# Kernel tuning notes

Hardware: AMD Instinct MI355X
Metric: run time of the kernel (lower is better)

The kernel has to match this reference:

```python
import jax, jax.numpy as jnp
import numpy as np

ALPHA = 0.5      # GCN2Conv alpha
THETA = 1.0      # GCN2Conv theta (beta_l = log(theta/l + 1))
EPS = 1e-5       # pyg LayerNorm eps
N_LAYERS = 8
N, E, DIN, DHID, DOUT = 50000, 800000, 128, 256, 128


def setup_inputs() -> dict:
    key = jax.random.key(0)
    ks = jax.random.split(key, 10)
    x = jax.random.normal(ks[0], (N, DIN), jnp.float32)
    edge_index = jax.random.randint(ks[1], (2, E), 0, N, dtype=jnp.int32)
    lin1_w = jax.random.normal(ks[2], (DIN, DHID), jnp.float32) / np.sqrt(DIN)
    lin1_b = jnp.zeros((DHID,), jnp.float32)
    conv_w1 = jax.random.normal(ks[3], (N_LAYERS, DHID, DHID), jnp.float32) / np.sqrt(DHID)
    conv_w2 = jax.random.normal(ks[4], (N_LAYERS, DHID, DHID), jnp.float32) / np.sqrt(DHID)
    norm_gamma = jnp.ones((N_LAYERS, DHID), jnp.float32)
    norm_beta = jnp.zeros((N_LAYERS, DHID), jnp.float32)
    lin2_w = jax.random.normal(ks[5], (DHID, DOUT), jnp.float32) / np.sqrt(DHID)
    lin2_b = jnp.zeros((DOUT,), jnp.float32)
    return {"x": x, "edge_index": edge_index, "lin1_w": lin1_w, "lin1_b": lin1_b,
            "conv_w1": conv_w1, "conv_w2": conv_w2, "norm_gamma": norm_gamma,
            "norm_beta": norm_beta, "lin2_w": lin2_w, "lin2_b": lin2_b}


def _gcn_norm(edge_index, n_nodes, dtype):
    # add self loops, then symmetric deg^{-1/2} A_hat deg^{-1/2} normalization
    loop = jnp.arange(n_nodes, dtype=edge_index.dtype)
    row = jnp.concatenate([edge_index[0], loop])
    col = jnp.concatenate([edge_index[1], loop])
    deg = jax.ops.segment_sum(jnp.ones_like(row, dtype=dtype), col, num_segments=n_nodes)
    dis = jnp.where(deg > 0, jax.lax.rsqrt(jnp.maximum(deg, 1e-12)), 0.0)
    return row, col, dis[row] * dis[col]


def _graph_layernorm(h, gamma, beta):
    # pyg LayerNorm mode='graph', batch=None: normalize over all nodes+features
    z = h - jnp.mean(h)
    z = z / (jnp.sqrt(jnp.mean(z * z)) + EPS)
    return gamma * z + beta


def reference(x, edge_index, lin1_w, lin1_b, conv_w1, conv_w2, norm_gamma, norm_beta, lin2_w, lin2_b):
    n_nodes = x.shape[0]
    row, col, enorm = _gcn_norm(edge_index, n_nodes, x.dtype)
    # lin1 + relu (dropout p=0 -> identity); residual=None -> zeros
    x0 = jax.nn.relu(x @ lin1_w + lin1_b)
    h = x0
    for i in range(conv_w1.shape[0]):
        beta_l = float(np.log(THETA / (i + 1) + 1.0))
        # sparse neighborhood aggregation: out[c] += norm * h[r]
        agg = jax.ops.segment_sum(h[row] * enorm[:, None], col, num_segments=n_nodes)
        t = (1.0 - ALPHA) * agg          # propagated part
        r = ALPHA * x0                   # initial-residual part (res = x0 + zeros)
        # shared_weights=False: separate weights for propagated and residual parts
        h = (1.0 - beta_l) * (t + r) + beta_l * (t @ conv_w1[i] + r @ conv_w2[i])
        h = jax.nn.relu(_graph_layernorm(h, norm_gamma[i], norm_beta[i]))
    return jax.nn.relu(h @ lin2_w + lin2_b)
```

## Files before the change

kernel.cpp:

```cpp
#include <hip/hip_runtime.h>
#include <hip/hip_bf16.h>
#include <math.h>

#define DIN 128
#define DH 256
#define DOUT 128
#define NLAYERS 8
#define EPSLN 1e-5f

typedef __hip_bfloat16 bf16;
typedef __attribute__((ext_vector_type(8))) short short8;
typedef __attribute__((ext_vector_type(4))) short short4v;
typedef __attribute__((ext_vector_type(4))) float f32x4;

__device__ __forceinline__ float ldf(const void* p, size_t idx, int isbf) {
    if (isbf) return __bfloat162float(((const bf16*)p)[idx]);
    return ((const float*)p)[idx];
}
__device__ __forceinline__ short f2s(float v) {
    bf16 b = __float2bfloat16(v);
    return *reinterpret_cast<short*>(&b);
}
__device__ __forceinline__ float s2f(short s) {
    unsigned int u = ((unsigned int)(unsigned short)s) << 16;
    float f;
    __builtin_memcpy(&f, &u, 4);
    return f;
}
__device__ __forceinline__ void gl_lds16(const void* g, void* l) {
    __builtin_amdgcn_global_load_lds(
        (const __attribute__((address_space(1))) unsigned int*)g,
        (__attribute__((address_space(3))) unsigned int*)l,
        16, 0, 0);
}

__global__ void k_detect(const unsigned int* __restrict__ xw, int* __restrict__ flag) {
    __shared__ int cnt;
    if (threadIdx.x == 0) cnt = 0;
    __syncthreads();
    unsigned int w = xw[threadIdx.x];
    int e = (w >> 7) & 0xFF;
    if (e >= 112 && e <= 140) atomicAdd(&cnt, 1);
    __syncthreads();
    if (threadIdx.x == 0) *flag = (cnt >= 128) ? 1 : 0;
}

__global__ void k_init_cnt(int* __restrict__ cnt, int N) {
    int i = blockIdx.x * blockDim.x + threadIdx.x;
    if (i < N) cnt[i] = 0;
}
__global__ void k_count(const int* __restrict__ cols, int* __restrict__ cnt, int E) {
    int e = blockIdx.x * blockDim.x + threadIdx.x;
    if (e < E) atomicAdd(&cnt[cols[e]], 1);
}
__global__ void k_dis(const int* __restrict__ cnt, float* __restrict__ dis, int N) {
    int i = blockIdx.x * blockDim.x + threadIdx.x;
    if (i < N) dis[i] = rsqrtf(1.0f + (float)cnt[i]);
}
__global__ void k_scan1(const int* __restrict__ cnt, int* __restrict__ rowptr,
                        int* __restrict__ bsum, int N) {
    __shared__ int s[256];
    int t = threadIdx.x;
    int i = blockIdx.x * 256 + t;
    s[t] = (i < N) ? cnt[i] : 0;
    __syncthreads();
    for (int off = 1; off < 256; off <<= 1) {
        int x = (t >= off) ? s[t - off] : 0;
        __syncthreads();
        s[t] += x;
        __syncthreads();
    }
    if (i < N) rowptr[i + 1] = s[t];
    if (t == 255) bsum[blockIdx.x] = s[255];
}
__global__ void k_scan2(int* __restrict__ bsum, int nb) {
    __shared__ int s[256];
    int t = threadIdx.x;
    s[t] = (t < nb) ? bsum[t] : 0;
    __syncthreads();
    for (int off = 1; off < 256; off <<= 1) {
        int x = (t >= off) ? s[t - off] : 0;
        __syncthreads();
        s[t] += x;
        __syncthreads();
    }
    if (t < nb) bsum[t] = s[t];
}
__global__ void k_scan3(int* __restrict__ rowptr, const int* __restrict__ bsum, int N) {
    int i = blockIdx.x * 256 + threadIdx.x;
    if (i == 0) rowptr[0] = 0;
    if (i < N && blockIdx.x > 0) rowptr[i + 1] += bsum[blockIdx.x - 1];
}
__global__ void k_cursor(const int* __restrict__ rowptr, int* __restrict__ cursor, int N) {
    int i = blockIdx.x * 256 + threadIdx.x;
    if (i < N) cursor[i] = rowptr[i];
}
__global__ void k_fill(const int* __restrict__ rows, const int* __restrict__ cols,
                       int* __restrict__ cursor, int* __restrict__ csr, int E) {
    int e = blockIdx.x * blockDim.x + threadIdx.x;
    if (e < E) {
        int c = cols[e], r = rows[e];
        int pos = atomicAdd(&cursor[c], 1);
        csr[pos] = r;
    }
}

__global__ void k_zero_stats(float* __restrict__ stats) {
    int t = threadIdx.x;
    if (t < 16) stats[t] = 0.0f;
}

__global__ void k_transw2(const void* __restrict__ w1, const void* __restrict__ w2,
                          const int* __restrict__ flag, short* __restrict__ wt) {
    __shared__ float tile[32][33];
    int z = blockIdx.z;
    int lay = z >> 1, m = z & 1;
    const void* src = m ? w2 : w1;
    size_t sbase = (size_t)lay * 65536;
    short* dst = wt + (size_t)lay * 131072 + (size_t)m * 256;
    float bl = logf(1.0f / (float)(lay + 1) + 1.0f);
    float c0 = 0.5f * (1.0f - bl);
    float c1 = 0.5f * bl;
    int isbf = *flag;
    int tx = threadIdx.x, ty = threadIdx.y;
    int n0 = blockIdx.x * 32, k0 = blockIdx.y * 32;
    #pragma unroll
    for (int i = 0; i < 4; i++) {
        int k = k0 + ty + i * 8;
        tile[ty + i * 8][tx] = ldf(src, sbase + (size_t)k * 256 + n0 + tx, isbf);
    }
    __syncthreads();
    #pragma unroll
    for (int i = 0; i < 4; i++) {
        int n = n0 + ty + i * 8;
        int k = k0 + tx;
        float v = c1 * tile[tx][ty + i * 8];
        if (k == n) v += c0;
        dst[(size_t)n * 512 + k] = f2s(v);
    }
}

__global__ void k_transw_lin(const void* __restrict__ src, const int* __restrict__ flag,
                             short* __restrict__ dst, int K, int Nc) {
    __shared__ float tile[32][33];
    int isbf = *flag;
    int tx = threadIdx.x, ty = threadIdx.y;
    int n0 = blockIdx.x * 32, k0 = blockIdx.y * 32;
    #pragma unroll
    for (int i = 0; i < 4; i++) {
        int k = k0 + ty + i * 8;
        tile[ty + i * 8][tx] = ldf(src, (size_t)k * Nc + n0 + tx, isbf);
    }
    __syncthreads();
    #pragma unroll
    for (int i = 0; i < 4; i++) {
        int n = n0 + ty + i * 8;
        dst[(size_t)n * K + k0 + tx] = f2s(tile[tx][ty + i * 8]);
    }
}

__global__ void k_convx(const void* __restrict__ x, const int* __restrict__ flag,
                        short* __restrict__ xb, int total) {
    int i = blockIdx.x * 256 + threadIdx.x;
    if (i < total) xb[i] = f2s(ldf(x, i, *flag));
}

template<int KK, int FINAL>
__global__ __launch_bounds__(256) void gemm_mfma(
    const short* __restrict__ A, const short* __restrict__ wt,
    const void* __restrict__ bias, const int* __restrict__ flag,
    void* __restrict__ outp, int Nn)
{
    __shared__ __align__(16) short Atile[128 * 32];
    __shared__ __align__(16) short Btile[128 * 32];
    int t = threadIdx.x;
    int w = t >> 6, lane = t & 63;
    int lr = lane & 15, quad = lane >> 4;
    int row0 = blockIdx.x * 128;
    int col0 = blockIdx.y * 128;
    int ncols = gridDim.y * 128;
    int sub = t & 3;
    int srow = t >> 2;
    f32x4 acc[2][8];
    #pragma unroll
    for (int m = 0; m < 2; m++)
        #pragma unroll
        for (int nt = 0; nt < 8; nt++)
            #pragma unroll
            for (int j = 0; j < 4; j++) acc[m][nt][j] = 0.f;

    for (int kb = 0; kb < KK; kb += 32) {
        #pragma unroll
        for (int r = 0; r < 2; r++) {
            int gr = row0 + srow + r * 64;
            if (gr >= Nn) gr = Nn - 1;
            gl_lds16(A + (size_t)gr * KK + kb + sub * 8,
                     Atile + (size_t)(t + r * 256) * 8);
        }
        #pragma unroll
        for (int r = 0; r < 2; r++) {
            int n = col0 + srow + r * 64;
            gl_lds16(wt + (size_t)n * KK + kb + sub * 8,
                     Btile + (size_t)(t + r * 256) * 8);
        }
        __syncthreads();
        short8 a0 = *(const short8*)(Atile + (w * 32 + lr) * 32 + quad * 8);
        short8 a1 = *(const short8*)(Atile + (w * 32 + 16 + lr) * 32 + quad * 8);
        #pragma unroll
        for (int nt = 0; nt < 8; nt++) {
            short8 bv = *(const short8*)(Btile + (nt * 16 + lr) * 32 + quad * 8);
            acc[0][nt] = __builtin_amdgcn_mfma_f32_16x16x32_bf16(a0, bv, acc[0][nt], 0, 0, 0);
            acc[1][nt] = __builtin_amdgcn_mfma_f32_16x16x32_bf16(a1, bv, acc[1][nt], 0, 0, 0);
        }
        __syncthreads();
    }
    const int isbf = *flag;
    #pragma unroll
    for (int m = 0; m < 2; m++) {
        #pragma unroll
        for (int nt = 0; nt < 8; nt++) {
            int gc = col0 + nt * 16 + lr;
            float bb = ldf(bias, gc, isbf);
            #pragma unroll
            for (int i = 0; i < 4; i++) {
                int gr = row0 + w * 32 + m * 16 + quad * 4 + i;
                if (gr < Nn) {
                    float v = acc[m][nt][i] + bb;
                    v = v > 0.f ? v : 0.f;
                    size_t off = (size_t)gr * ncols + gc;
                    if (FINAL) {
                        if (isbf) ((bf16*)outp)[off] = __float2bfloat16(v);
                        else      ((float*)outp)[off] = v;
                    } else {
                        ((bf16*)outp)[off] = __float2bfloat16(v);
                    }
                }
            }
        }
    }
}

__global__ __launch_bounds__(256) void k_gather4(
    const int* __restrict__ rowptr, const int* __restrict__ csr,
    const float* __restrict__ dis, const bf16* __restrict__ hsrc,
    bf16* __restrict__ agg, int N)
{
    int gid = blockIdx.x * 256 + threadIdx.x;
    int node = gid >> 6;
    if (node >= N) return;
    int col = (gid & 63) * 4;
    const short* hs = (const short*)hsrc;
    float dc = dis[node];
    float a0[4], a1[4], a2[4], a3[4];
    {
        short4v hv = *(const short4v*)(hs + (size_t)node * DH + col);
        #pragma unroll
        for (int j = 0; j < 4; j++) {
            a0[j] = dc * s2f(hv[j]);
            a1[j] = 0.f; a2[j] = 0.f; a3[j] = 0.f;
        }
    }
    int i = rowptr[node], e1 = rowptr[node + 1];
    for (; i + 8 <= e1; i += 8) {
        int r0 = csr[i],     r1 = csr[i + 1], r2 = csr[i + 2], r3 = csr[i + 3];
        int r4 = csr[i + 4], r5 = csr[i + 5], r6 = csr[i + 6], r7 = csr[i + 7];
        float w0 = dis[r0], w1 = dis[r1], w2 = dis[r2], w3 = dis[r3];
        float w4 = dis[r4], w5 = dis[r5], w6 = dis[r6], w7 = dis[r7];
        short4v v0 = *(const short4v*)(hs + (size_t)r0 * DH + col);
        short4v v1 = *(const short4v*)(hs + (size_t)r1 * DH + col);
        short4v v2 = *(const short4v*)(hs + (size_t)r2 * DH + col);
        short4v v3 = *(const short4v*)(hs + (size_t)r3 * DH + col);
        short4v v4 = *(const short4v*)(hs + (size_t)r4 * DH + col);
        short4v v5 = *(const short4v*)(hs + (size_t)r5 * DH + col);
        short4v v6 = *(const short4v*)(hs + (size_t)r6 * DH + col);
        short4v v7 = *(const short4v*)(hs + (size_t)r7 * DH + col);
        #pragma unroll
        for (int j = 0; j < 4; j++) {
            a0[j] = fmaf(w0, s2f(v0[j]), a0[j]);
            a1[j] = fmaf(w1, s2f(v1[j]), a1[j]);
            a2[j] = fmaf(w2, s2f(v2[j]), a2[j]);
            a3[j] = fmaf(w3, s2f(v3[j]), a3[j]);
            a0[j] = fmaf(w4, s2f(v4[j]), a0[j]);
            a1[j] = fmaf(w5, s2f(v5[j]), a1[j]);
            a2[j] = fmaf(w6, s2f(v6[j]), a2[j]);
            a3[j] = fmaf(w7, s2f(v7[j]), a3[j]);
        }
    }
    for (; i + 2 <= e1; i += 2) {
        int r0 = csr[i], r1 = csr[i + 1];
        float w0 = dis[r0], w1 = dis[r1];
        short4v v0 = *(const short4v*)(hs + (size_t)r0 * DH + col);
        short4v v1 = *(const short4v*)(hs + (size_t)r1 * DH + col);
        #pragma unroll
        for (int j = 0; j < 4; j++) {
            a0[j] = fmaf(w0, s2f(v0[j]), a0[j]);
            a1[j] = fmaf(w1, s2f(v1[j]), a1[j]);
        }
    }
    for (; i < e1; i++) {
        int r = csr[i];
        float wr = dis[r];
        short4v v0 = *(const short4v*)(hs + (size_t)r * DH + col);
        #pragma unroll
        for (int j = 0; j < 4; j++) a0[j] = fmaf(wr, s2f(v0[j]), a0[j]);
    }
    short4v o;
    #pragma unroll
    for (int j = 0; j < 4; j++) o[j] = f2s(dc * ((a0[j] + a1[j]) + (a2[j] + a3[j])));
    *(short4v*)((short*)agg + (size_t)node * DH + col) = o;
}

__global__ __launch_bounds__(256) void gemm_layer4(
    const bf16* __restrict__ agg, const bf16* __restrict__ x0,
    const short* __restrict__ wt, bf16* __restrict__ h,
    float* __restrict__ stats2, int Nn)
{
    __shared__ __align__(16) short Atile[128 * 32];
    __shared__ __align__(16) short Btile[128 * 32];
    __shared__ float red[512];
    int t = threadIdx.x;
    int w = t >> 6, lane = t & 63;
    int lr = lane & 15, quad = lane >> 4;
    int row0 = blockIdx.x * 128;
    int col0 = blockIdx.y * 128;
    int sub = t & 3;
    int srow = t >> 2;
    f32x4 acc[2][8];
    #pragma unroll
    for (int m = 0; m < 2; m++)
        #pragma unroll
        for (int nt = 0; nt < 8; nt++)
            #pragma unroll
            for (int j = 0; j < 4; j++) acc[m][nt][j] = 0.f;

    for (int kb = 0; kb < 512; kb += 32) {
        const short* Asrc = (const short*)((kb < DH) ? agg : x0);
        int ka = kb & (DH - 1);
        #pragma unroll
        for (int r = 0; r < 2; r++) {
            int gr = row0 + srow + r * 64;
            if (gr >= Nn) gr = Nn - 1;
            gl_lds16(Asrc + (size_t)gr * DH + ka + sub * 8,
                     Atile + (size_t)(t + r * 256) * 8);
        }
        #pragma unroll
        for (int r = 0; r < 2; r++) {
            int n = col0 + srow + r * 64;
            gl_lds16(wt + (size_t)n * 512 + kb + sub * 8,
                     Btile + (size_t)(t + r * 256) * 8);
        }
        __syncthreads();
        short8 a0 = *(const short8*)(Atile + (w * 32 + lr) * 32 + quad * 8);
        short8 a1 = *(const short8*)(Atile + (w * 32 + 16 + lr) * 32 + quad * 8);
        #pragma unroll
        for (int nt = 0; nt < 8; nt++) {
            short8 bv = *(const short8*)(Btile + (nt * 16 + lr) * 32 + quad * 8);
            acc[0][nt] = __builtin_amdgcn_mfma_f32_16x16x32_bf16(a0, bv, acc[0][nt], 0, 0, 0);
            acc[1][nt] = __builtin_amdgcn_mfma_f32_16x16x32_bf16(a1, bv, acc[1][nt], 0, 0, 0);
        }
        __syncthreads();
    }
    float lsum = 0.f, lsq = 0.f;
    #pragma unroll
    for (int m = 0; m < 2; m++) {
        #pragma unroll
        for (int nt = 0; nt < 8; nt++) {
            int gc = col0 + nt * 16 + lr;
            #pragma unroll
            for (int i = 0; i < 4; i++) {
                int gr = row0 + w * 32 + m * 16 + quad * 4 + i;
                if (gr < Nn) {
                    float v = acc[m][nt][i];
                    h[(size_t)gr * DH + gc] = __float2bfloat16(v);
                    lsum += v;
                    lsq += v * v;
                }
            }
        }
    }
    red[t] = lsum;
    red[256 + t] = lsq;
    __syncthreads();
    for (int s = 128; s > 0; s >>= 1) {
        if (t < s) { red[t] += red[t + s]; red[256 + t] += red[256 + t + s]; }
        __syncthreads();
    }
    if (t == 0) {
        atomicAdd(&stats2[0], red[0]);
        atomicAdd(&stats2[1], red[256]);
    }
}

__global__ __launch_bounds__(256) void k_applyT(
    bf16* __restrict__ h, const float* __restrict__ stats2, float invTotal,
    const void* __restrict__ g, const void* __restrict__ b, size_t loff,
    const int* __restrict__ flag, int total)
{
    int idx = blockIdx.x * 256 + threadIdx.x;
    if (idx >= total) return;
    const int isbf = *flag;
    float mu = stats2[0] * invTotal;
    float var = stats2[1] * invTotal - mu * mu;
    var = var > 0.f ? var : 0.f;
    float inv = 1.0f / (sqrtf(var) + EPSLN);
    int j = idx & (DH - 1);
    float gg = ldf(g, loff + j, isbf);
    float bb = ldf(b, loff + j, isbf);
    float v = fmaf(gg * inv, __bfloat162float(h[idx]), fmaf(-gg * inv, mu, bb));
    v = v > 0.f ? v : 0.f;
    h[idx] = __float2bfloat16(v);
}

extern "C" void kernel_launch(void* const* d_in, const int* in_sizes, int n_in,
                              void* d_out, int out_size, void* d_ws, size_t ws_size,
                              hipStream_t stream) {
    const void* x      = d_in[0];
    const int*  ei     = (const int*)d_in[1];
    const void* lin1_w = d_in[2];
    const void* lin1_b = d_in[3];
    const void* conv_w1= d_in[4];
    const void* conv_w2= d_in[5];
    const void* gam    = d_in[6];
    const void* bet    = d_in[7];
    const void* lin2_w = d_in[8];
    const void* lin2_b = d_in[9];

    const int N = in_sizes[0] / DIN;
    const int E = in_sizes[1] / 2;
    const int* rows = ei;
    const int* cols = ei + E;
    const size_t NDH = (size_t)N * DH;
    const size_t Nr = ((size_t)N + 255) / 256 * 256;

    char* p = (char*)d_ws;
    auto alloc = [&](size_t bytes) { char* q = p; p += (bytes + 255) & ~(size_t)255; return q; };
    float* dis    = (float*)alloc(Nr * 4);
    float* stats  = (float*)alloc(1024);
    int*   flag   = (int*)(stats + 16);
    int*   cnt    = (int*)alloc(Nr * 4);
    int*   rowptr = (int*)alloc((Nr + 256) * 4);
    int*   cursor = (int*)alloc(Nr * 4);
    int*   bsum   = (int*)alloc(1024);
    int*   csr    = (int*)alloc((size_t)E * 4);
    short* wt     = (short*)alloc((size_t)NLAYERS * 131072 * 2);
    short* w1t    = (short*)alloc((size_t)DH * DIN * 2);
    short* w2t    = (short*)alloc((size_t)DOUT * DH * 2);
    short* xb     = (short*)alloc((size_t)N * DIN * 2);
    bf16*  agg    = (bf16*)alloc(NDH * 2);
    bf16*  x0     = (bf16*)alloc(NDH * 2);
    bf16*  h      = (bf16*)alloc(NDH * 2);

    dim3 blk(256);
    int nbN = (N + 255) / 256;
    dim3 gN(nbN);
    dim3 gE((E + 255) / 256);
    dim3 gB128_2((N + 127) / 128, 2);
    dim3 gB128_1((N + 127) / 128, 1);
    dim3 gG((N + 3) / 4);
    dim3 gElem((unsigned)((NDH + 255) / 256));
    dim3 gTW(8, 8, 16);
    dim3 bTW(32, 8);

    k_detect<<<1, 256, 0, stream>>>((const unsigned int*)x, flag);
    k_init_cnt<<<gN, blk, 0, stream>>>(cnt, N);
    k_count<<<gE, blk, 0, stream>>>(cols, cnt, E);
    k_dis<<<gN, blk, 0, stream>>>(cnt, dis, N);
    k_scan1<<<gN, blk, 0, stream>>>(cnt, rowptr, bsum, N);
    k_scan2<<<1, 256, 0, stream>>>(bsum, nbN);
    k_scan3<<<gN, blk, 0, stream>>>(rowptr, bsum, N);
    k_cursor<<<gN, blk, 0, stream>>>(rowptr, cursor, N);
    k_fill<<<gE, blk, 0, stream>>>(rows, cols, cursor, csr, E);
    k_zero_stats<<<1, 64, 0, stream>>>(stats);
    k_transw2<<<gTW, bTW, 0, stream>>>(conv_w1, conv_w2, flag, wt);
    k_transw_lin<<<dim3(DH / 32, DIN / 32), bTW, 0, stream>>>(lin1_w, flag, w1t, DIN, DH);
    k_transw_lin<<<dim3(DOUT / 32, DH / 32), bTW, 0, stream>>>(lin2_w, flag, w2t, DH, DOUT);
    k_convx<<<dim3((unsigned)(((size_t)N * DIN + 255) / 256)), blk, 0, stream>>>(x, flag, xb, N * DIN);

    gemm_mfma<DIN, 0><<<gB128_2, blk, 0, stream>>>(xb, w1t, lin1_b, flag, x0, N);

    const float invTotal = 1.0f / ((float)N * (float)DH);
    for (int l = 0; l < NLAYERS; l++) {
        const bf16* hsrc = (l == 0) ? x0 : h;
        if (l > 0) {
            k_applyT<<<gElem, blk, 0, stream>>>(h, stats + 2 * (l - 1), invTotal,
                                                gam, bet, (size_t)(l - 1) * DH,
                                                flag, (int)NDH);
        }
        k_gather4<<<gG, blk, 0, stream>>>(rowptr, csr, dis, hsrc, agg, N);
        gemm_layer4<<<gB128_2, blk, 0, stream>>>(agg, x0, wt + (size_t)l * 131072,
                                                 h, stats + 2 * l, N);
    }
    k_applyT<<<gElem, blk, 0, stream>>>(h, stats + 2 * (NLAYERS - 1), invTotal,
                                        gam, bet, (size_t)(NLAYERS - 1) * DH,
                                        flag, (int)NDH);
    gemm_mfma<DH, 1><<<gB128_1, blk, 0, stream>>>((const short*)h, w2t, lin2_b,
                                                  flag, d_out, N);
}
```

Baseline: 1.329 ms.

## Fuse graph LayerNorm+ReLU into gather and final GEMM, drop apply pass

Removes the separate k_applyT elementwise pass over h. The LayerNorm affine and ReLU are now applied on the fly to each neighbor row read in the gather kernel, and while loading A tiles in the final GEMM. It also merges the cursor init into scan3 and the stats zeroing into init_cnt, cutting launches. The catch is that normalization is recomputed for every edge read (about 17 per node) instead of once per element. The final GEMM also switches from async global-to-LDS loads to register loads with per-element gamma/beta fetches.

```diff
diff --git a/kernel.cpp b/kernel.cpp
--- a/kernel.cpp
+++ b/kernel.cpp
@@ -45,9 +45,10 @@
     if (threadIdx.x == 0) *flag = (cnt >= 128) ? 1 : 0;
 }
 
-__global__ void k_init_cnt(int* __restrict__ cnt, int N) {
+__global__ void k_init_cnt(int* __restrict__ cnt, float* __restrict__ stats, int N) {
     int i = blockIdx.x * blockDim.x + threadIdx.x;
     if (i < N) cnt[i] = 0;
+    if (blockIdx.x == 0 && threadIdx.x < 16) stats[threadIdx.x] = 0.0f;
 }
 __global__ void k_count(const int* __restrict__ cols, int* __restrict__ cnt, int E) {
     int e = blockIdx.x * blockDim.x + threadIdx.x;
@@ -86,14 +87,15 @@
     }
     if (t < nb) bsum[t] = s[t];
 }
-__global__ void k_scan3(int* __restrict__ rowptr, const int* __restrict__ bsum, int N) {
+__global__ void k_scan3(int* __restrict__ rowptr, const int* __restrict__ bsum,
+                        int* __restrict__ cursor, int N) {
     int i = blockIdx.x * 256 + threadIdx.x;
-    if (i == 0) rowptr[0] = 0;
-    if (i < N && blockIdx.x > 0) rowptr[i + 1] += bsum[blockIdx.x - 1];
-}
-__global__ void k_cursor(const int* __restrict__ rowptr, int* __restrict__ cursor, int N) {
-    int i = blockIdx.x * 256 + threadIdx.x;
-    if (i < N) cursor[i] = rowptr[i];
+    if (i == 0) { rowptr[0] = 0; cursor[0] = 0; }
+    if (i < N) {
+        int v = rowptr[i + 1] + ((blockIdx.x > 0) ? bsum[blockIdx.x - 1] : 0);
+        rowptr[i + 1] = v;
+        cursor[i + 1] = v;
+    }
 }
 __global__ void k_fill(const int* __restrict__ rows, const int* __restrict__ cols,
                        int* __restrict__ cursor, int* __restrict__ csr, int E) {
@@ -103,11 +105,6 @@
         int pos = atomicAdd(&cursor[c], 1);
         csr[pos] = r;
     }
-}
-
-__global__ void k_zero_stats(float* __restrict__ stats) {
-    int t = threadIdx.x;
-    if (t < 16) stats[t] = 0.0f;
 }
 
 __global__ void k_transw2(const void* __restrict__ w1, const void* __restrict__ w2,
@@ -165,10 +162,12 @@
     if (i < total) xb[i] = f2s(ldf(x, i, *flag));
 }
 
-template<int KK, int FINAL>
+template<int KK, int FINAL, int TRANSA>
 __global__ __launch_bounds__(256) void gemm_mfma(
     const short* __restrict__ A, const short* __restrict__ wt,
     const void* __restrict__ bias, const int* __restrict__ flag,
+    const void* __restrict__ g, const void* __restrict__ b, size_t loff,
+    const float* __restrict__ stats2, float invTotal,
     void* __restrict__ outp, int Nn)
 {
     __shared__ __align__(16) short Atile[128 * 32];
@@ -181,6 +180,14 @@
     int ncols = gridDim.y * 128;
     int sub = t & 3;
     int srow = t >> 2;
+    const int isbf = *flag;
+    float mu = 0.f, inv = 0.f;
+    if (TRANSA) {
+        mu = stats2[0] * invTotal;
+        float var = stats2[1] * invTotal - mu * mu;
+        var = var > 0.f ? var : 0.f;
+        inv = 1.0f / (sqrtf(var) + EPSLN);
+    }
     f32x4 acc[2][8];
     #pragma unroll
     for (int m = 0; m < 2; m++)
@@ -194,8 +201,23 @@
         for (int r = 0; r < 2; r++) {
             int gr = row0 + srow + r * 64;
             if (gr >= Nn) gr = Nn - 1;
-            gl_lds16(A + (size_t)gr * KK + kb + sub * 8,
-                     Atile + (size_t)(t + r * 256) * 8);
+            if (TRANSA) {
+                short8 av = *(const short8*)(A + (size_t)gr * KK + kb + sub * 8);
+                short8 tv;
+                #pragma unroll
+                for (int j = 0; j < 8; j++) {
+                    int kc = kb + sub * 8 + j;
+                    float gg = ldf(g, loff + kc, isbf);
+                    float bb = ldf(b, loff + kc, isbf);
+                    float v = fmaf(gg * inv, s2f(av[j]), fmaf(-gg * inv, mu, bb));
+                    v = v > 0.f ? v : 0.f;
+                    tv[j] = f2s(v);
+                }
+                *(short8*)(Atile + (size_t)(t + r * 256) * 8) = tv;
+            } else {
+                gl_lds16(A + (size_t)gr * KK + kb + sub * 8,
+                         Atile + (size_t)(t + r * 256) * 8);
+            }
         }
         #pragma unroll
         for (int r = 0; r < 2; r++) {
@@ -214,7 +236,6 @@
         }
         __syncthreads();
     }
-    const int isbf = *flag;
     #pragma unroll
     for (int m = 0; m < 2; m++) {
         #pragma unroll
@@ -240,15 +261,36 @@
     }
 }
 
-__global__ __launch_bounds__(256) void k_gather4(
+__global__ __launch_bounds__(256) void k_gather5(
     const int* __restrict__ rowptr, const int* __restrict__ csr,
     const float* __restrict__ dis, const bf16* __restrict__ hsrc,
-    bf16* __restrict__ agg, int N)
+    bf16* __restrict__ agg,
+    const void* __restrict__ g, const void* __restrict__ b, size_t loff,
+    const float* __restrict__ stats2, float invTotal, int useLN,
+    const int* __restrict__ flag, int N)
 {
     int gid = blockIdx.x * 256 + threadIdx.x;
     int node = gid >> 6;
     if (node >= N) return;
     int col = (gid & 63) * 4;
+    float cA[4], cB[4];
+    if (useLN) {
+        int isbf = *flag;
+        float mu = stats2[0] * invTotal;
+        float var = stats2[1] * invTotal - mu * mu;
+        var = var > 0.f ? var : 0.f;
+        float inv = 1.0f / (sqrtf(var) + EPSLN);
+        #pragma unroll
+        for (int j = 0; j < 4; j++) {
+            float gg = ldf(g, loff + col + j, isbf);
+            float bb = ldf(b, loff + col + j, isbf);
+            cA[j] = gg * inv;
+            cB[j] = fmaf(-gg * inv, mu, bb);
+        }
+    } else {
+        #pragma unroll
+        for (int j = 0; j < 4; j++) { cA[j] = 1.0f; cB[j] = 0.0f; }
+    }
     const short* hs = (const short*)hsrc;
     float dc = dis[node];
     float a0[4], a1[4], a2[4], a3[4];
@@ -256,7 +298,9 @@
         short4v hv = *(const short4v*)(hs + (size_t)node * DH + col);
         #pragma unroll
         for (int j = 0; j < 4; j++) {
-            a0[j] = dc * s2f(hv[j]);
+            float v = fmaf(cA[j], s2f(hv[j]), cB[j]);
+            v = v > 0.f ? v : 0.f;
+            a0[j] = dc * v;
             a1[j] = 0.f; a2[j] = 0.f; a3[j] = 0.f;
         }
     }
@@ -276,14 +320,22 @@
         short4v v7 = *(const short4v*)(hs + (size_t)r7 * DH + col);
         #pragma unroll
         for (int j = 0; j < 4; j++) {
-            a0[j] = fmaf(w0, s2f(v0[j]), a0[j]);
-            a1[j] = fmaf(w1, s2f(v1[j]), a1[j]);
-            a2[j] = fmaf(w2, s2f(v2[j]), a2[j]);
-            a3[j] = fmaf(w3, s2f(v3[j]), a3[j]);
-            a0[j] = fmaf(w4, s2f(v4[j]), a0[j]);
-            a1[j] = fmaf(w5, s2f(v5[j]), a1[j]);
-            a2[j] = fmaf(w6, s2f(v6[j]), a2[j]);
-            a3[j] = fmaf(w7, s2f(v7[j]), a3[j]);
+            float t0 = fmaf(cA[j], s2f(v0[j]), cB[j]); t0 = t0 > 0.f ? t0 : 0.f;
+            float t1 = fmaf(cA[j], s2f(v1[j]), cB[j]); t1 = t1 > 0.f ? t1 : 0.f;
+            float t2 = fmaf(cA[j], s2f(v2[j]), cB[j]); t2 = t2 > 0.f ? t2 : 0.f;
+            float t3 = fmaf(cA[j], s2f(v3[j]), cB[j]); t3 = t3 > 0.f ? t3 : 0.f;
+            float t4 = fmaf(cA[j], s2f(v4[j]), cB[j]); t4 = t4 > 0.f ? t4 : 0.f;
+            float t5 = fmaf(cA[j], s2f(v5[j]), cB[j]); t5 = t5 > 0.f ? t5 : 0.f;
+            float t6 = fmaf(cA[j], s2f(v6[j]), cB[j]); t6 = t6 > 0.f ? t6 : 0.f;
+            float t7 = fmaf(cA[j], s2f(v7[j]), cB[j]); t7 = t7 > 0.f ? t7 : 0.f;
+            a0[j] = fmaf(w0, t0, a0[j]);
+            a1[j] = fmaf(w1, t1, a1[j]);
+            a2[j] = fmaf(w2, t2, a2[j]);
+            a3[j] = fmaf(w3, t3, a3[j]);
+            a0[j] = fmaf(w4, t4, a0[j]);
+            a1[j] = fmaf(w5, t5, a1[j]);
+            a2[j] = fmaf(w6, t6, a2[j]);
+            a3[j] = fmaf(w7, t7, a3[j]);
         }
     }
     for (; i + 2 <= e1; i += 2) {
@@ -293,8 +345,10 @@
         short4v v1 = *(const short4v*)(hs + (size_t)r1 * DH + col);
         #pragma unroll
         for (int j = 0; j < 4; j++) {
-            a0[j] = fmaf(w0, s2f(v0[j]), a0[j]);
-            a1[j] = fmaf(w1, s2f(v1[j]), a1[j]);
+            float t0 = fmaf(cA[j], s2f(v0[j]), cB[j]); t0 = t0 > 0.f ? t0 : 0.f;
+            float t1 = fmaf(cA[j], s2f(v1[j]), cB[j]); t1 = t1 > 0.f ? t1 : 0.f;
+            a0[j] = fmaf(w0, t0, a0[j]);
+            a1[j] = fmaf(w1, t1, a1[j]);
         }
     }
     for (; i < e1; i++) {
@@ -302,7 +356,10 @@
         float wr = dis[r];
         short4v v0 = *(const short4v*)(hs + (size_t)r * DH + col);
         #pragma unroll
-        for (int j = 0; j < 4; j++) a0[j] = fmaf(wr, s2f(v0[j]), a0[j]);
+        for (int j = 0; j < 4; j++) {
+            float t0 = fmaf(cA[j], s2f(v0[j]), cB[j]); t0 = t0 > 0.f ? t0 : 0.f;
+            a0[j] = fmaf(wr, t0, a0[j]);
+        }
     }
     short4v o;
     #pragma unroll
@@ -391,26 +448,6 @@
     }
 }
 
-__global__ __launch_bounds__(256) void k_applyT(
-    bf16* __restrict__ h, const float* __restrict__ stats2, float invTotal,
-    const void* __restrict__ g, const void* __restrict__ b, size_t loff,
-    const int* __restrict__ flag, int total)
-{
-    int idx = blockIdx.x * 256 + threadIdx.x;
-    if (idx >= total) return;
-    const int isbf = *flag;
-    float mu = stats2[0] * invTotal;
-    float var = stats2[1] * invTotal - mu * mu;
-    var = var > 0.f ? var : 0.f;
-    float inv = 1.0f / (sqrtf(var) + EPSLN);
-    int j = idx & (DH - 1);
-    float gg = ldf(g, loff + j, isbf);
-    float bb = ldf(b, loff + j, isbf);
-    float v = fmaf(gg * inv, __bfloat162float(h[idx]), fmaf(-gg * inv, mu, bb));
-    v = v > 0.f ? v : 0.f;
-    h[idx] = __float2bfloat16(v);
-}
-
 extern "C" void kernel_launch(void* const* d_in, const int* in_sizes, int n_in,
                               void* d_out, int out_size, void* d_ws, size_t ws_size,
                               hipStream_t stream) {
@@ -439,7 +476,7 @@
     int*   flag   = (int*)(stats + 16);
     int*   cnt    = (int*)alloc(Nr * 4);
     int*   rowptr = (int*)alloc((Nr + 256) * 4);
-    int*   cursor = (int*)alloc(Nr * 4);
+    int*   cursor = (int*)alloc((Nr + 256) * 4);
     int*   bsum   = (int*)alloc(1024);
     int*   csr    = (int*)alloc((size_t)E * 4);
     short* wt     = (short*)alloc((size_t)NLAYERS * 131072 * 2);
@@ -457,42 +494,39 @@
     dim3 gB128_2((N + 127) / 128, 2);
     dim3 gB128_1((N + 127) / 128, 1);
     dim3 gG((N + 3) / 4);
-    dim3 gElem((unsigned)((NDH + 255) / 256));
     dim3 gTW(8, 8, 16);
     dim3 bTW(32, 8);
 
     k_detect<<<1, 256, 0, stream>>>((const unsigned int*)x, flag);
-    k_init_cnt<<<gN, blk, 0, stream>>>(cnt, N);
+    k_init_cnt<<<gN, blk, 0, stream>>>(cnt, stats, N);
     k_count<<<gE, blk, 0, stream>>>(cols, cnt, E);
     k_dis<<<gN, blk, 0, stream>>>(cnt, dis, N);
     k_scan1<<<gN, blk, 0, stream>>>(cnt, rowptr, bsum, N);
     k_scan2<<<1, 256, 0, stream>>>(bsum, nbN);
-    k_scan3<<<gN, blk, 0, stream>>>(rowptr, bsum, N);
-    k_cursor<<<gN, blk, 0, stream>>>(rowptr, cursor, N);
+    k_scan3<<<gN, blk, 0, stream>>>(rowptr, bsum, cursor, N);
     k_fill<<<gE, blk, 0, stream>>>(rows, cols, cursor, csr, E);
-    k_zero_stats<<<1, 64, 0, stream>>>(stats);
     k_transw2<<<gTW, bTW, 0, stream>>>(conv_w1, conv_w2, flag, wt);
     k_transw_lin<<<dim3(DH / 32, DIN / 32), bTW, 0, stream>>>(lin1_w, flag, w1t, DIN, DH);
     k_transw_lin<<<dim3(DOUT / 32, DH / 32), bTW, 0, stream>>>(lin2_w, flag, w2t, DH, DOUT);
     k_convx<<<dim3((unsigned)(((size_t)N * DIN + 255) / 256)), blk, 0, stream>>>(x, flag, xb, N * DIN);
 
-    gemm_mfma<DIN, 0><<<gB128_2, blk, 0, stream>>>(xb, w1t, lin1_b, flag, x0, N);
+    gemm_mfma<DIN, 0, 0><<<gB128_2, blk, 0, stream>>>(xb, w1t, lin1_b, flag,
+                                                      nullptr, nullptr, 0, stats, 0.f,
+                                                      x0, N);
 
     const float invTotal = 1.0f / ((float)N * (float)DH);
     for (int l = 0; l < NLAYERS; l++) {
         const bf16* hsrc = (l == 0) ? x0 : h;
-        if (l > 0) {
-            k_applyT<<<gElem, blk, 0, stream>>>(h, stats + 2 * (l - 1), invTotal,
-                                                gam, bet, (size_t)(l - 1) * DH,
-                                                flag, (int)NDH);
-        }
-        k_gather4<<<gG, blk, 0, stream>>>(rowptr, csr, dis, hsrc, agg, N);
+        size_t loff = (l == 0) ? 0 : (size_t)(l - 1) * DH;
+        const float* st = (l == 0) ? stats : stats + 2 * (l - 1);
+        k_gather5<<<gG, blk, 0, stream>>>(rowptr, csr, dis, hsrc, agg,
+                                          gam, bet, loff, st, invTotal,
+                                          l > 0 ? 1 : 0, flag, N);
         gemm_layer4<<<gB128_2, blk, 0, stream>>>(agg, x0, wt + (size_t)l * 131072,
                                                  h, stats + 2 * l, N);
     }
-    k_applyT<<<gElem, blk, 0, stream>>>(h, stats + 2 * (NLAYERS - 1), invTotal,
-                                        gam, bet, (size_t)(NLAYERS - 1) * DH,
-                                        flag, (int)NDH);
-    gemm_mfma<DH, 1><<<gB128_1, blk, 0, stream>>>((const short*)h, w2t, lin2_b,
-                                                  flag, d_out, N);
-}
+    gemm_mfma<DH, 1, 1><<<gB128_1, blk, 0, stream>>>((const short*)h, w2t, lin2_b, flag,
+                                                     gam, bet, (size_t)(NLAYERS - 1) * DH,
+                                                     stats + 2 * (NLAYERS - 1), invTotal,
+                                                     d_out, N);
+}
```

New measurement: 1.280 ms. -3.7%, faster.
